# Performance work log

Measured on AMD Instinct MI355X. Metric: run time of the kernel, lower is better.

The kernel has to match this reference:

```python
import jax, jax.numpy as jnp
import numpy as np
from jax import lax

TEMP = 1e-5       # CustomConv2d.temp
K_ITERS = 10      # perform_clustering num_iterations


def _unfold3(x):
    # F.unfold(kernel=3, pad=1, stride=1): (N,C,H,W) -> (N, C*9, H*W), feature order (c, ki, kj)
    N, C, H, W = x.shape
    xp = jnp.pad(x, ((0, 0), (0, 0), (1, 1), (1, 1)))
    pats = jnp.stack([xp[:, :, i:i + H, j:j + W] for i in range(3) for j in range(3)], axis=2)  # (N,C,9,H,W)
    return pats.reshape(N, C * 9, H * W)


def _fold3(patches, C, H):
    # F.fold(output_size=(3H,3H), kernel=3, stride=3, pad=1): non-overlapping tiling.
    # Block (bi,bj), offset (ki,kj) lands at pixel (3*bi-1+ki, 3*bj-1+kj); row/col -1 is cut,
    # rows/cols 3H-1 (and 3H-2 col edge handled by grid extent) are zero-filled.
    N = patches.shape[0]
    grid = patches.reshape(N, C, 3, 3, H, H).transpose(0, 1, 4, 2, 5, 3).reshape(N, C, 3 * H, 3 * H)
    return jnp.pad(grid[:, :, 1:, 1:], ((0, 0), (0, 0), (0, 1), (0, 1)))


def _cdist(a, b):
    # Euclidean distance matrix (E,K) = torch.cdist(a,b)
    d2 = jnp.sum(a * a, axis=1)[:, None] - 2.0 * (a @ b.T) + jnp.sum(b * b, axis=1)[None, :]
    return jnp.sqrt(jnp.maximum(d2, 0.0))


def _kmeans(flat, centers):
    K = centers.shape[0]
    ones = jnp.ones((flat.shape[0],), flat.dtype)

    def body(c, _):
        labels = jnp.argmin(_cdist(flat, c), axis=1)
        sums = jax.ops.segment_sum(flat, labels, num_segments=K)
        cnt = jax.ops.segment_sum(ones, labels, num_segments=K)
        new = jnp.where(cnt[:, None] > 0, sums / jnp.maximum(cnt, 1.0)[:, None], c)
        return new, None

    centers, _ = lax.scan(body, centers, None, length=K_ITERS)
    return centers


def _custom_conv(x, w, b, center_idx):
    N, C, H, W = x.shape
    this_patch = _unfold3(x)                         # (N, C*9, H*W)
    D = C * 9
    # clustering operates on detached patches (torch .detach()); note the original's
    # view(-1, D) row-major chunking is reproduced exactly by reshape(-1, D)
    flat_sg = lax.stop_gradient(this_patch).reshape(-1, D)
    centers = _kmeans(flat_sg, flat_sg[center_idx])  # (K, D)
    # soft quantization (gradient flows through this path)
    flat = this_patch.reshape(-1, D)
    dist = _cdist(flat, centers)
    soft = jax.nn.softmax(-dist * TEMP, axis=1)
    trans = soft @ centers
    final = (TEMP / (TEMP + 1.0)) * trans + (1.0 / (TEMP + 1.0)) * flat
    x_dash = _fold3(final.reshape(this_patch.shape), C, H)   # (N, C, 3H, 3H)
    out = lax.conv_general_dilated(x_dash, w, (3, 3), ((1, 1), (1, 1)),
                                   dimension_numbers=('NCHW', 'OIHW', 'NCHW'))
    return out + b[None, :, None, None]


def _pool(x):
    return lax.reduce_window(x, -jnp.inf, lax.max, (1, 1, 2, 2), (1, 1, 2, 2), 'VALID')


def _forward(x, conv1_w, conv1_b, conv2_w, conv2_b, fc_w, fc_b, idx1, idx2):
    h = _pool(jax.nn.relu(_custom_conv(x, conv1_w, conv1_b, idx1)))   # (N,16,14,14)
    h = _pool(jax.nn.relu(_custom_conv(h, conv2_w, conv2_b, idx2)))   # (N,32,7,7)
    h = h.reshape(h.shape[0], -1)
    return h @ fc_w.T + fc_b


def setup_inputs() -> dict:
    key = jax.random.key(0)
    ks = jax.random.split(key, 9)
    N, K = 512, 128
    return {
        'x': jax.random.normal(ks[0], (N, 1, 28, 28), jnp.float32),
        'conv1_w': jax.random.normal(ks[1], (16, 1, 3, 3), jnp.float32) * 0.1,
        'conv1_b': jax.random.normal(ks[2], (16,), jnp.float32) * 0.1,
        'conv2_w': jax.random.normal(ks[3], (32, 16, 3, 3), jnp.float32) * 0.05,
        'conv2_b': jax.random.normal(ks[4], (32,), jnp.float32) * 0.1,
        'fc_w': jax.random.normal(ks[5], (10, 32 * 7 * 7), jnp.float32) * 0.02,
        'fc_b': jax.random.normal(ks[6], (10,), jnp.float32) * 0.02,
        'center_idx1': jax.random.randint(ks[7], (K,), 0, N * 784),
        'center_idx2': jax.random.randint(ks[8], (K,), 0, N * 196),
    }


def reference(x, conv1_w, conv1_b, conv2_w, conv2_b, fc_w, fc_b, center_idx1, center_idx2):
    return _forward(x, conv1_w, conv1_b, conv2_w, conv2_b, fc_w, fc_b, center_idx1, center_idx2)
```

## Files before the change

kernel.cpp:

```cpp
#include <hip/hip_runtime.h>


typedef __fp16 h2v __attribute__((ext_vector_type(2)));
typedef __fp16 h8  __attribute__((ext_vector_type(8)));
typedef float  f4  __attribute__((ext_vector_type(4)));

__device__ __forceinline__ unsigned as_u32(h2v h) {
    union { unsigned u; h2v h; } x; x.h = h; return x.u;
}
__device__ __forceinline__ h8 ld_h8(const unsigned* p) {
    union { uint4 u; h8 h; } v; v.u = *(const uint4*)p; return v.h;
}

__global__ __launch_bounds__(256, 2) void fused_cnn(
    const float* __restrict__ x,
    const float* __restrict__ w1,
    const float* __restrict__ b1,
    const float* __restrict__ w2,
    const float* __restrict__ b2,
    const float* __restrict__ fcw,
    const float* __restrict__ fcb,
    float* __restrict__ out)
{
    const int n = blockIdx.x;
    const int t = threadIdx.x;
    const float s = (float)(1.0 / 1.00001);

    __shared__ float    uni[32 * 197];
    __shared__ unsigned sh1[2 * 18 * 16 * 4];
    __shared__ unsigned swr[32 * 80];
    __shared__ float    sh2[1568];
    __shared__ float    sred[10][4];

    float*    sx  = uni;
    unsigned* raw = (unsigned*)(uni + 1080);
    float*    Dl  = uni;

    for (int i = t; i < 1080; i += 256) sx[i] = 0.0f;
    for (int i = t; i < 2304; i += 256) sh1[i] = 0u;
    if (t < 196) {
        const float4 v = ((const float4*)(x + n * 784))[t];
        const int r = t / 7, c4 = (t - r * 7) * 4;
        float* dst = &sx[(r + 1) * 36 + c4 + 1];
        dst[0] = v.x; dst[1] = v.y; dst[2] = v.z; dst[3] = v.w;
    }
    {
        uint4* rawv = (uint4*)raw;
        const uint4* w2v = (const uint4*)w2;
        for (int i = t; i < 1152; i += 256) rawv[i] = w2v[i];
    }
    if (t < 256) {
        const int oc = t >> 3;
        swr[oc * 80 + 72 + (t & 7)] = 0u;
    }
    __syncthreads();

    for (int i = t; i < 2304; i += 256) {
        const int oc = i / 72, r = i - oc * 72;
        const int ki = r / 24, r2 = r - ki * 24, kj = r2 >> 3, c = 2 * (r2 & 7);
        const float a = __uint_as_float(raw[(oc * 16 + c) * 9 + ki * 3 + kj]);
        const float b = __uint_as_float(raw[(oc * 16 + c + 1) * 9 + ki * 3 + kj]);
        swr[oc * 80 + r] = as_u32(__builtin_amdgcn_cvt_pkrtz(a, b));
    }
    {
        const int ocp = t & 7;
        float wa[9], wb[9];
        #pragma unroll
        for (int k = 0; k < 9; ++k) { wa[k] = w1[ocp * 18 + k]; wb[k] = w1[ocp * 18 + 9 + k]; }
        const float ba = b1[2 * ocp], bb = b1[2 * ocp + 1];
        const int cg = ocp >> 2, slot = ocp & 3;

        for (int p = t >> 3; p < 98; p += 32) {
            const int row = p / 7;
            const int pcp = p - row * 7;
            float pr[4][6];
            const float* base = &sx[(2 * row) * 36 + 4 * pcp];
            #pragma unroll
            for (int rr = 0; rr < 4; ++rr) {
                const float4 a4 = *(const float4*)(base + rr * 36);
                const float2 a2 = *(const float2*)(base + rr * 36 + 4);
                pr[rr][0] = a4.x; pr[rr][1] = a4.y; pr[rr][2] = a4.z; pr[rr][3] = a4.w;
                pr[rr][4] = a2.x; pr[rr][5] = a2.y;
            }
            float va[2][4], vb[2][4];
            #pragma unroll
            for (int cr = 0; cr < 2; ++cr)
                #pragma unroll
                for (int cc = 0; cc < 4; ++cc) {
                    float a = 0.0f, b = 0.0f;
                    #pragma unroll
                    for (int ki = 0; ki < 3; ++ki)
                        #pragma unroll
                        for (int kj = 0; kj < 3; ++kj) {
                            const float pv = pr[cr + ki][cc + kj];
                            a = fmaf(wa[ki * 3 + kj], pv, a);
                            b = fmaf(wb[ki * 3 + kj], pv, b);
                        }
                    va[cr][cc] = a; vb[cr][cc] = b;
                }
            #pragma unroll
            for (int d = 0; d < 2; ++d) {
                const float ma = fmaxf(fmaxf(va[0][2 * d], va[0][2 * d + 1]),
                                       fmaxf(va[1][2 * d], va[1][2 * d + 1]));
                const float mb = fmaxf(fmaxf(vb[0][2 * d], vb[0][2 * d + 1]),
                                       fmaxf(vb[1][2 * d], vb[1][2 * d + 1]));
                const float pa = fmaxf(fmaf(s, ma, ba), 0.0f);
                const float pb = fmaxf(fmaf(s, mb, bb), 0.0f);
                const int xc = 2 * pcp + d + 1;
                sh1[((cg * 18 + row + 1) * 16 + xc) * 4 + slot] =
                    as_u32(__builtin_amdgcn_cvt_pkrtz(pa, pb));
            }
        }
    }
    __syncthreads();

    {
        const int lane = t & 63, wv = t >> 6;
        const int l15 = lane & 15, kgrp = lane >> 4;
        h8 afr[2][5];
        #pragma unroll
        for (int m = 0; m < 2; ++m)
            #pragma unroll
            for (int ss = 0; ss < 5; ++ss)
                afr[m][ss] = ld_h8(&swr[(m * 16 + l15) * 80 + 16 * ss + 4 * kgrp]);

        const int khi = kgrp >> 1, cgl = kgrp & 1;
        for (int nt = wv; nt < 13; nt += 4) {
            const int p = 16 * nt + l15;
            const int y = p / 14, x2 = p - 14 * y;
            h8 bfr[5];
            #pragma unroll
            for (int ss = 0; ss < 5; ++ss) {
                const int tt = 2 * ss + khi;
                const int ki = tt / 3, kj = tt - 3 * ki;
                const int g = (cgl * 18 + y + ki) * 16 + (x2 + kj);
                bfr[ss] = ld_h8(&sh1[g * 4]);
            }
            f4 d0 = {0.f, 0.f, 0.f, 0.f}, d1 = {0.f, 0.f, 0.f, 0.f};
            #pragma unroll
            for (int ss = 0; ss < 5; ++ss) {
                d0 = __builtin_amdgcn_mfma_f32_16x16x32_f16(afr[0][ss], bfr[ss], d0, 0, 0, 0);
                d1 = __builtin_amdgcn_mfma_f32_16x16x32_f16(afr[1][ss], bfr[ss], d1, 0, 0, 0);
            }
            if (p < 196) {
                #pragma unroll
                for (int r = 0; r < 4; ++r) {
                    Dl[(kgrp * 4 + r) * 197 + p]      = d0[r];
                    Dl[(16 + kgrp * 4 + r) * 197 + p] = d1[r];
                }
            }
        }
    }
    __syncthreads();

    for (int item = t; item < 1568; item += 256) {
        const int oc = item / 49, q = item - oc * 49;
        const int py = q / 7, px = q - py * 7;
        const float* dp = &Dl[oc * 197 + 28 * py + 2 * px];
        const float m = fmaxf(fmaxf(dp[0], dp[1]), fmaxf(dp[14], dp[15]));
        sh2[item] = fmaxf(fmaf(s, m, b2[oc]), 0.0f);
    }
    __syncthreads();

    float part[10];
    #pragma unroll
    for (int j = 0; j < 10; ++j) part[j] = 0.0f;
    const float4* sh2v = (const float4*)sh2;
    const float4* fcwv = (const float4*)fcw;
    for (int i = t; i < 392; i += 256) {
        const float4 h = sh2v[i];
        #pragma unroll
        for (int j = 0; j < 10; ++j) {
            const float4 wq = fcwv[j * 392 + i];
            part[j] = fmaf(h.x, wq.x, fmaf(h.y, wq.y,
                      fmaf(h.z, wq.z, fmaf(h.w, wq.w, part[j]))));
        }
    }
    #pragma unroll
    for (int j = 0; j < 10; ++j) {
        float vsum = part[j];
        #pragma unroll
        for (int off = 32; off > 0; off >>= 1) vsum += __shfl_down(vsum, off);
        if ((t & 63) == 0) sred[j][t >> 6] = vsum;
    }
    __syncthreads();
    if (t < 10)
        out[n * 10 + t] = sred[t][0] + sred[t][1] + sred[t][2] + sred[t][3] + fcb[t];
}

extern "C" void kernel_launch(void* const* d_in, const int* in_sizes, int n_in,
                              void* d_out, int out_size, void* d_ws, size_t ws_size,
                              hipStream_t stream) {
    const float* x   = (const float*)d_in[0];
    const float* w1  = (const float*)d_in[1];
    const float* b1  = (const float*)d_in[2];
    const float* w2  = (const float*)d_in[3];
    const float* b2  = (const float*)d_in[4];
    const float* fcw = (const float*)d_in[5];
    const float* fcb = (const float*)d_in[6];
    float* out = (float*)d_out;

    fused_cnn<<<512, 256, 0, stream>>>(x, w1, b1, w2, b2, fcw, fcb, out);
}
```

Before: 16.28 us.

## Transpose conv2 output layout, pad weight rows, restructure FC reduction per wave

Stores the MFMA conv2 accumulators as pixel-major rows of 40 floats written with vector f4 stores, instead of scattered scalar stores into a channel-major layout. The weight fragment stride is padded from 80 to 84 words, presumably to reduce LDS bank conflicts. conv2 bias is staged into shared memory. The FC layer now gives each wave whole output classes and reduces with shuffles, removing the cross-wave shared-memory reduction and its final barrier. The pooling stage now does strided reads across the transposed layout, which may conflict in LDS, and the shared-memory footprint grows.

```diff
diff --git a/kernel.cpp b/kernel.cpp
--- a/kernel.cpp
+++ b/kernel.cpp
@@ -26,11 +26,11 @@
     const int t = threadIdx.x;
     const float s = (float)(1.0 / 1.00001);
 
-    __shared__ float    uni[32 * 197];
+    __shared__ float    uni[208 * 40];
     __shared__ unsigned sh1[2 * 18 * 16 * 4];
-    __shared__ unsigned swr[32 * 80];
+    __shared__ unsigned swr[32 * 84];
     __shared__ float    sh2[1568];
-    __shared__ float    sred[10][4];
+    __shared__ float    sb2[32];
 
     float*    sx  = uni;
     unsigned* raw = (unsigned*)(uni + 1080);
@@ -49,10 +49,11 @@
         const uint4* w2v = (const uint4*)w2;
         for (int i = t; i < 1152; i += 256) rawv[i] = w2v[i];
     }
-    if (t < 256) {
+    {
         const int oc = t >> 3;
-        swr[oc * 80 + 72 + (t & 7)] = 0u;
+        swr[oc * 84 + 72 + (t & 7)] = 0u;
     }
+    if (t < 32) sb2[t] = b2[t];
     __syncthreads();
 
     for (int i = t; i < 2304; i += 256) {
@@ -60,7 +61,7 @@
         const int ki = r / 24, r2 = r - ki * 24, kj = r2 >> 3, c = 2 * (r2 & 7);
         const float a = __uint_as_float(raw[(oc * 16 + c) * 9 + ki * 3 + kj]);
         const float b = __uint_as_float(raw[(oc * 16 + c + 1) * 9 + ki * 3 + kj]);
-        swr[oc * 80 + r] = as_u32(__builtin_amdgcn_cvt_pkrtz(a, b));
+        swr[oc * 84 + r] = as_u32(__builtin_amdgcn_cvt_pkrtz(a, b));
     }
     {
         const int ocp = t & 7;
@@ -122,7 +123,7 @@
         for (int m = 0; m < 2; ++m)
             #pragma unroll
             for (int ss = 0; ss < 5; ++ss)
-                afr[m][ss] = ld_h8(&swr[(m * 16 + l15) * 80 + 16 * ss + 4 * kgrp]);
+                afr[m][ss] = ld_h8(&swr[(m * 16 + l15) * 84 + 16 * ss + 4 * kgrp]);
 
         const int khi = kgrp >> 1, cgl = kgrp & 1;
         for (int nt = wv; nt < 13; nt += 4) {
@@ -142,13 +143,8 @@
                 d0 = __builtin_amdgcn_mfma_f32_16x16x32_f16(afr[0][ss], bfr[ss], d0, 0, 0, 0);
                 d1 = __builtin_amdgcn_mfma_f32_16x16x32_f16(afr[1][ss], bfr[ss], d1, 0, 0, 0);
             }
-            if (p < 196) {
-                #pragma unroll
-                for (int r = 0; r < 4; ++r) {
-                    Dl[(kgrp * 4 + r) * 197 + p]      = d0[r];
-                    Dl[(16 + kgrp * 4 + r) * 197 + p] = d1[r];
-                }
-            }
+            *(f4*)(&Dl[p * 40 + kgrp * 4])      = d0;
+            *(f4*)(&Dl[p * 40 + kgrp * 4 + 16]) = d1;
         }
     }
     __syncthreads();
@@ -156,36 +152,30 @@
     for (int item = t; item < 1568; item += 256) {
         const int oc = item / 49, q = item - oc * 49;
         const int py = q / 7, px = q - py * 7;
-        const float* dp = &Dl[oc * 197 + 28 * py + 2 * px];
-        const float m = fmaxf(fmaxf(dp[0], dp[1]), fmaxf(dp[14], dp[15]));
-        sh2[item] = fmaxf(fmaf(s, m, b2[oc]), 0.0f);
+        const int p0 = 28 * py + 2 * px;
+        const float m = fmaxf(fmaxf(Dl[p0 * 40 + oc],        Dl[(p0 + 1) * 40 + oc]),
+                              fmaxf(Dl[(p0 + 14) * 40 + oc], Dl[(p0 + 15) * 40 + oc]));
+        sh2[item] = fmaxf(fmaf(s, m, sb2[oc]), 0.0f);
     }
     __syncthreads();
 
-    float part[10];
-    #pragma unroll
-    for (int j = 0; j < 10; ++j) part[j] = 0.0f;
-    const float4* sh2v = (const float4*)sh2;
-    const float4* fcwv = (const float4*)fcw;
-    for (int i = t; i < 392; i += 256) {
-        const float4 h = sh2v[i];
-        #pragma unroll
-        for (int j = 0; j < 10; ++j) {
-            const float4 wq = fcwv[j * 392 + i];
-            part[j] = fmaf(h.x, wq.x, fmaf(h.y, wq.y,
-                      fmaf(h.z, wq.z, fmaf(h.w, wq.w, part[j]))));
+    {
+        const int wv = t >> 6, lane = t & 63;
+        const float4* sh2v = (const float4*)sh2;
+        const float4* fcwv = (const float4*)fcw;
+        for (int j = wv; j < 10; j += 4) {
+            float part = 0.0f;
+            for (int i = lane; i < 392; i += 64) {
+                const float4 h  = sh2v[i];
+                const float4 wq = fcwv[j * 392 + i];
+                part = fmaf(h.x, wq.x, fmaf(h.y, wq.y,
+                       fmaf(h.z, wq.z, fmaf(h.w, wq.w, part))));
+            }
+            #pragma unroll
+            for (int off = 32; off > 0; off >>= 1) part += __shfl_down(part, off);
+            if (lane == 0) out[n * 10 + j] = part + fcb[j];
         }
     }
-    #pragma unroll
-    for (int j = 0; j < 10; ++j) {
-        float vsum = part[j];
-        #pragma unroll
-        for (int off = 32; off > 0; off >>= 1) vsum += __shfl_down(vsum, off);
-        if ((t & 63) == 0) sred[j][t >> 6] = vsum;
-    }
-    __syncthreads();
-    if (t < 10)
-        out[n * 10 + t] = sred[t][0] + sred[t][1] + sred[t][2] + sred[t][3] + fcb[t];
 }
 
 extern "C" void kernel_launch(void* const* d_in, const int* in_sizes, int n_in,
```

Result: slower. 17.82 us (+9.5%).
